# Performance work log

Measured on AMD Instinct MI355X. Metric: run time of the kernel, lower is better.

Reference implementation:

```python
import jax, jax.numpy as jnp
import numpy as np

MARGIN = 1.0  # config['margin']


def setup_inputs() -> dict:
    key = jax.random.key(0)
    k1, k2 = jax.random.split(key)
    features = jax.random.normal(k1, (1024, 512), dtype=jnp.float32)
    labels = jax.random.randint(k2, (1024,), 0, 32)
    return {"features": features, "labels": labels}


def _cdist(x):
    # Pairwise euclidean distances, matching torch.cdist; zero-distance
    # entries (e.g., the diagonal) get zero gradient like torch's backward.
    sq = jnp.sum(x * x, axis=-1)
    d2 = sq[:, None] + sq[None, :] - 2.0 * (x @ x.T)
    d2 = jnp.maximum(d2, 0.0)
    safe = jnp.where(d2 > 0.0, d2, 1.0)
    return jnp.where(d2 > 0.0, jnp.sqrt(safe), 0.0)


def reference(features, labels):
    n = features.shape[0]
    dist = _cdist(features)                                   # [N, N]
    pos = (labels[:, None] == labels[None, :]).astype(features.dtype)  # includes diagonal, as in the torch code
    neg = 1.0 - pos

    # loss = sum_i sum_{p in pos(i)} sum_{k in neg(i)} relu(d[i,p] - d[i,k] + margin)
    # Stream over anchors i to avoid materializing the [N, N, N] broadcast.
    def per_anchor(args):
        di, pi, ni = args  # each [N]
        t = jax.nn.relu(di[:, None] - di[None, :] + MARGIN)   # [N_pos_axis, N_neg_axis]
        return jnp.sum(t * (pi[:, None] * ni[None, :]))

    losses = jax.lax.map(per_anchor, (dist, pos, neg))        # [N]
    return jnp.sum(losses) / (n + 1e-8)
```

## Files before the change

### kernel.cpp

```cpp
#include <hip/hip_runtime.h>
#include <math.h>

#define MARGIN 1.0f

typedef short short8 __attribute__((ext_vector_type(8)));
typedef unsigned short ushort8 __attribute__((ext_vector_type(8)));
typedef float floatx16 __attribute__((ext_vector_type(16)));

typedef const __attribute__((address_space(1))) void g_void;
typedef __attribute__((address_space(3))) void s_void;

__device__ inline unsigned short bf16_rne(float x) {
  unsigned u = __float_as_uint(x);
  unsigned r = (u + 0x7FFF + ((u >> 16) & 1)) >> 16;
  return (unsigned short)r;
}
__device__ inline float bf16_to_f32(unsigned short h) {
  return __uint_as_float(((unsigned)h) << 16);
}

__global__ __launch_bounds__(64) void conv_kernel(
    const float* __restrict__ f, unsigned short* __restrict__ fhi,
    unsigned short* __restrict__ flo, float* __restrict__ sq, int N, int D) {
  const int r = blockIdx.x;
  const int t = threadIdx.x;
  float acc = 0.f;
  if (t * 8 < D) {
    const float* src = f + (size_t)r * D + t * 8;
    float4 v0 = *(const float4*)(src);
    float4 v1 = *(const float4*)(src + 4);
    float xs[8] = {v0.x, v0.y, v0.z, v0.w, v1.x, v1.y, v1.z, v1.w};
    ushort8 hs, ls;
#pragma unroll
    for (int e = 0; e < 8; ++e) {
      float x = xs[e];
      acc += x * x;
      unsigned short h = bf16_rne(x);
      hs[e] = h;
      ls[e] = bf16_rne(x - bf16_to_f32(h));
    }
    const size_t off = ((size_t)t * N + r) * 8;
    *(ushort8*)(fhi + off) = hs;
    *(ushort8*)(flo + off) = ls;
  }
  for (int off = 32; off > 0; off >>= 1) acc += __shfl_down(acc, off, 64);
  if (t == 0) sq[r] = acc;
}

__global__ __launch_bounds__(256) void dist_kernel(
    const unsigned short* __restrict__ fhi, const unsigned short* __restrict__ flo,
    const float* __restrict__ sqv, float* __restrict__ dist, int N, int D) {
  __shared__ ushort8 T[2][4][8][64];

  const int tid = threadIdx.x;
  const int w = tid >> 6;
  const int lane = tid & 63;
  const int rowBase = blockIdx.y * 64;
  const int colBase = blockIdx.x * 64;

  const unsigned short* srcs[4] = {fhi, flo, fhi, flo};
  const int bases[4] = {rowBase, rowBase, colBase, colBase};

  const int wr = (w >> 1) * 32;
  const int wc = (w & 1) * 32;
  const int m = lane & 31;
  const int h = lane >> 5;

  auto issueLoads = [&](int k0, int bb) {
    const int c0 = k0 >> 3;
#pragma unroll
    for (int s = 0; s < 8; ++s) {
      const int a = s >> 1;
      const int c = (w << 1) | (s & 1);
      const unsigned short* gp =
          srcs[a] + ((size_t)(c0 + c) * N + bases[a] + lane) * 8;
      __builtin_amdgcn_global_load_lds((g_void*)gp, (s_void*)&T[bb][a][c][0],
                                       16, 0, 0);
    }
  };

  floatx16 acc = {};
  int b = 0;

  issueLoads(0, 0);
  __syncthreads();

  for (int k0 = 0; k0 < D; k0 += 64) {
    if (k0 + 64 < D) issueLoads(k0 + 64, b ^ 1);
#pragma unroll
    for (int kk = 0; kk < 4; ++kk) {
      const int c = 2 * kk + h;
      short8 ahf = *(const short8*)&T[b][0][c][wr + m];
      short8 alf = *(const short8*)&T[b][1][c][wr + m];
      short8 bhf = *(const short8*)&T[b][2][c][wc + m];
      short8 blf = *(const short8*)&T[b][3][c][wc + m];
      acc = __builtin_amdgcn_mfma_f32_32x32x16_bf16(ahf, bhf, acc, 0, 0, 0);
      acc = __builtin_amdgcn_mfma_f32_32x32x16_bf16(ahf, blf, acc, 0, 0, 0);
      acc = __builtin_amdgcn_mfma_f32_32x32x16_bf16(alf, bhf, acc, 0, 0, 0);
    }
    __syncthreads();
    b ^= 1;
  }

  const int col = colBase + wc + m;
  const float sqc = sqv[col];
#pragma unroll
  for (int r = 0; r < 16; ++r) {
    const int row = rowBase + wr + (r & 3) + 8 * (r >> 2) + 4 * h;
    float d2 = sqv[row] + sqc - 2.0f * acc[r];
    d2 = d2 > 0.f ? d2 : 0.f;
    dist[(size_t)row * N + col] = sqrtf(d2);
  }
}

__global__ __launch_bounds__(256) void anchor_loss_kernel(
    const float* __restrict__ dist, const int* __restrict__ labels,
    float* __restrict__ partial, int N) {
  const int i = blockIdx.x;
  const int tid = threadIdx.x;
  const int lane = tid & 63;

  __shared__ float dpos[1024];
  __shared__ float dneg[1024];
  __shared__ int cnt[2];
  __shared__ float red[4];

  if (tid < 2) cnt[tid] = 0;
  __syncthreads();

  const int lab = labels[i];
  const float* drow = dist + (size_t)i * N;

  for (int jb = 0; jb < N; jb += 256) {
    int j = jb + tid;
    float d = drow[j];
    bool isPos = (labels[j] == lab);

    unsigned long long mp = __ballot(isPos);
    unsigned long long mn = ~mp;
    unsigned long long lt = (1ull << lane) - 1ull;

    int base_p = 0, base_n = 0;
    if (lane == 0) {
      base_p = atomicAdd(&cnt[0], __popcll(mp));
      base_n = atomicAdd(&cnt[1], 64 - __popcll(mp));
    }
    base_p = __shfl(base_p, 0, 64);
    base_n = __shfl(base_n, 0, 64);

    if (isPos) dpos[base_p + __popcll(mp & lt)] = d + MARGIN;
    else       dneg[base_n + __popcll(mn & lt)] = d;
  }
  __syncthreads();

  const int np = cnt[0], nn = cnt[1];

  float dk[4];
#pragma unroll
  for (int e = 0; e < 4; ++e) {
    int k = tid + 256 * e;
    dk[e] = (k < nn) ? dneg[k] : 1e30f;
  }

  float accv = 0.f;
  for (int p = 0; p < np; ++p) {
    float t = dpos[p];
#pragma unroll
    for (int e = 0; e < 4; ++e) {
      float v = t - dk[e];
      accv += (v > 0.f) ? v : 0.f;
    }
  }

  for (int off = 32; off > 0; off >>= 1) accv += __shfl_down(accv, off, 64);
  if (lane == 0) red[tid >> 6] = accv;
  __syncthreads();
  if (tid == 0) partial[i] = red[0] + red[1] + red[2] + red[3];
}

__global__ __launch_bounds__(256) void final_reduce_kernel(
    const float* __restrict__ partial, float* __restrict__ out, int N) {
  float acc = 0.f;
  for (int j = threadIdx.x; j < N; j += 256) acc += partial[j];
  for (int off = 32; off > 0; off >>= 1) acc += __shfl_down(acc, off, 64);
  __shared__ float red[4];
  if ((threadIdx.x & 63) == 0) red[threadIdx.x >> 6] = acc;
  __syncthreads();
  if (threadIdx.x == 0) {
    double s = (double)red[0] + (double)red[1] + (double)red[2] + (double)red[3];
    out[0] = (float)(s / ((double)N + 1e-8));
  }
}

extern "C" void kernel_launch(void* const* d_in, const int* in_sizes, int n_in,
                              void* d_out, int out_size, void* d_ws, size_t ws_size,
                              hipStream_t stream) {
  const float* f = (const float*)d_in[0];
  const int* labels = (const int*)d_in[1];
  int N = in_sizes[1];
  int D = in_sizes[0] / N;
  float* out = (float*)d_out;

  unsigned short* fhi = (unsigned short*)d_ws;
  unsigned short* flo = fhi + (size_t)N * D;
  float* sq = (float*)(flo + (size_t)N * D);
  float* dist = sq + N;
  float* partial = dist + (size_t)N * N;

  conv_kernel<<<N, 64, 0, stream>>>(f, fhi, flo, sq, N, D);
  dim3 grid(N / 64, N / 64);
  dist_kernel<<<grid, 256, 0, stream>>>(fhi, flo, sq, dist, N, D);
  anchor_loss_kernel<<<N, 256, 0, stream>>>(dist, labels, partial, N);
  final_reduce_kernel<<<1, 256, 0, stream>>>(partial, out, N);
}
```

Measured before the change: 78.25 us.

## Fuse final reduction into anchor kernel, reshape conversion grid, split MFMA accumulators

The final reduction kernel is folded into the anchor loss kernel with a last-block atomic counter, which removes one launch. The counter is reset inside the conversion kernel. The conversion kernel now uses 16 blocks of 1024 threads, with each lane owning one row and a shared-memory reduction for the squared norms. The dist kernel splits its three MFMA chains into independent accumulators to break the dependency between them. The costs are more registers in the dist kernel and far fewer blocks in the conversion kernel, which may underfill the GPU.

```diff
diff --git a/kernel.cpp b/kernel.cpp
--- a/kernel.cpp
+++ b/kernel.cpp
@@ -19,14 +19,23 @@
   return __uint_as_float(((unsigned)h) << 16);
 }
 
-__global__ __launch_bounds__(64) void conv_kernel(
+__global__ __launch_bounds__(1024) void conv_kernel(
     const float* __restrict__ f, unsigned short* __restrict__ fhi,
-    unsigned short* __restrict__ flo, float* __restrict__ sq, int N, int D) {
-  const int r = blockIdx.x;
+    unsigned short* __restrict__ flo, float* __restrict__ sq,
+    int* __restrict__ counter, int N, int D) {
   const int t = threadIdx.x;
-  float acc = 0.f;
-  if (t * 8 < D) {
-    const float* src = f + (size_t)r * D + t * 8;
+  const int lane = t & 63;
+  const int cg = t >> 6;
+  const int row = blockIdx.x * 64 + lane;
+
+  if (blockIdx.x == 0 && t == 0) *counter = 0;
+
+  float partial = 0.f;
+#pragma unroll
+  for (int ci = 0; ci < 4; ++ci) {
+    const int c = cg * 4 + ci;
+    if (c * 8 >= D) break;
+    const float* src = f + (size_t)row * D + c * 8;
     float4 v0 = *(const float4*)(src);
     float4 v1 = *(const float4*)(src + 4);
     float xs[8] = {v0.x, v0.y, v0.z, v0.w, v1.x, v1.y, v1.z, v1.w};
@@ -34,17 +43,25 @@
 #pragma unroll
     for (int e = 0; e < 8; ++e) {
       float x = xs[e];
-      acc += x * x;
-      unsigned short h = bf16_rne(x);
-      hs[e] = h;
-      ls[e] = bf16_rne(x - bf16_to_f32(h));
-    }
-    const size_t off = ((size_t)t * N + r) * 8;
+      partial += x * x;
+      unsigned short hh = bf16_rne(x);
+      hs[e] = hh;
+      ls[e] = bf16_rne(x - bf16_to_f32(hh));
+    }
+    const size_t off = ((size_t)c * N + row) * 8;
     *(ushort8*)(fhi + off) = hs;
     *(ushort8*)(flo + off) = ls;
   }
-  for (int off = 32; off > 0; off >>= 1) acc += __shfl_down(acc, off, 64);
-  if (t == 0) sq[r] = acc;
+
+  __shared__ float sred[16][64];
+  sred[cg][lane] = partial;
+  __syncthreads();
+  if (cg == 0) {
+    float s = 0.f;
+#pragma unroll
+    for (int w2 = 0; w2 < 16; ++w2) s += sred[w2][lane];
+    sq[row] = s;
+  }
 }
 
 __global__ __launch_bounds__(256) void dist_kernel(
@@ -79,7 +96,7 @@
     }
   };
 
-  floatx16 acc = {};
+  floatx16 acc0 = {}, acc1 = {}, acc2 = {};
   int b = 0;
 
   issueLoads(0, 0);
@@ -94,9 +111,9 @@
       short8 alf = *(const short8*)&T[b][1][c][wr + m];
       short8 bhf = *(const short8*)&T[b][2][c][wc + m];
       short8 blf = *(const short8*)&T[b][3][c][wc + m];
-      acc = __builtin_amdgcn_mfma_f32_32x32x16_bf16(ahf, bhf, acc, 0, 0, 0);
-      acc = __builtin_amdgcn_mfma_f32_32x32x16_bf16(ahf, blf, acc, 0, 0, 0);
-      acc = __builtin_amdgcn_mfma_f32_32x32x16_bf16(alf, bhf, acc, 0, 0, 0);
+      acc0 = __builtin_amdgcn_mfma_f32_32x32x16_bf16(ahf, bhf, acc0, 0, 0, 0);
+      acc1 = __builtin_amdgcn_mfma_f32_32x32x16_bf16(ahf, blf, acc1, 0, 0, 0);
+      acc2 = __builtin_amdgcn_mfma_f32_32x32x16_bf16(alf, bhf, acc2, 0, 0, 0);
     }
     __syncthreads();
     b ^= 1;
@@ -107,7 +124,8 @@
 #pragma unroll
   for (int r = 0; r < 16; ++r) {
     const int row = rowBase + wr + (r & 3) + 8 * (r >> 2) + 4 * h;
-    float d2 = sqv[row] + sqc - 2.0f * acc[r];
+    float a = acc0[r] + acc1[r] + acc2[r];
+    float d2 = sqv[row] + sqc - 2.0f * a;
     d2 = d2 > 0.f ? d2 : 0.f;
     dist[(size_t)row * N + col] = sqrtf(d2);
   }
@@ -115,6 +133,7 @@
 
 __global__ __launch_bounds__(256) void anchor_loss_kernel(
     const float* __restrict__ dist, const int* __restrict__ labels,
+    int* __restrict__ counter, float* __restrict__ out,
     float* __restrict__ partial, int N) {
   const int i = blockIdx.x;
   const int tid = threadIdx.x;
@@ -124,6 +143,7 @@
   __shared__ float dneg[1024];
   __shared__ int cnt[2];
   __shared__ float red[4];
+  __shared__ int isLastS;
 
   if (tid < 2) cnt[tid] = 0;
   __syncthreads();
@@ -164,10 +184,10 @@
 
   float accv = 0.f;
   for (int p = 0; p < np; ++p) {
-    float t = dpos[p];
+    float tpos = dpos[p];
 #pragma unroll
     for (int e = 0; e < 4; ++e) {
-      float v = t - dk[e];
+      float v = tpos - dk[e];
       accv += (v > 0.f) ? v : 0.f;
     }
   }
@@ -175,18 +195,22 @@
   for (int off = 32; off > 0; off >>= 1) accv += __shfl_down(accv, off, 64);
   if (lane == 0) red[tid >> 6] = accv;
   __syncthreads();
-  if (tid == 0) partial[i] = red[0] + red[1] + red[2] + red[3];
-}
-
-__global__ __launch_bounds__(256) void final_reduce_kernel(
-    const float* __restrict__ partial, float* __restrict__ out, int N) {
+
+  if (tid == 0) {
+    partial[i] = red[0] + red[1] + red[2] + red[3];
+    __threadfence();
+    isLastS = (atomicAdd(counter, 1) == gridDim.x - 1);
+  }
+  __syncthreads();
+  if (!isLastS) return;
+
+  __threadfence();
   float acc = 0.f;
-  for (int j = threadIdx.x; j < N; j += 256) acc += partial[j];
+  for (int j = tid; j < N; j += 256) acc += partial[j];
   for (int off = 32; off > 0; off >>= 1) acc += __shfl_down(acc, off, 64);
-  __shared__ float red[4];
-  if ((threadIdx.x & 63) == 0) red[threadIdx.x >> 6] = acc;
-  __syncthreads();
-  if (threadIdx.x == 0) {
+  if (lane == 0) red[tid >> 6] = acc;
+  __syncthreads();
+  if (tid == 0) {
     double s = (double)red[0] + (double)red[1] + (double)red[2] + (double)red[3];
     out[0] = (float)(s / ((double)N + 1e-8));
   }
@@ -206,10 +230,10 @@
   float* sq = (float*)(flo + (size_t)N * D);
   float* dist = sq + N;
   float* partial = dist + (size_t)N * N;
-
-  conv_kernel<<<N, 64, 0, stream>>>(f, fhi, flo, sq, N, D);
+  int* counter = (int*)(partial + N);
+
+  conv_kernel<<<N / 64, 1024, 0, stream>>>(f, fhi, flo, sq, counter, N, D);
   dim3 grid(N / 64, N / 64);
   dist_kernel<<<grid, 256, 0, stream>>>(fhi, flo, sq, dist, N, D);
-  anchor_loss_kernel<<<N, 256, 0, stream>>>(dist, labels, partial, N);
-  final_reduce_kernel<<<1, 256, 0, stream>>>(partial, out, N);
-}
+  anchor_loss_kernel<<<N, 256, 0, stream>>>(dist, labels, counter, out, partial, N);
+}
```

Result: slower. 99.40 us (+27.0%).
